# Optimization experiments

Measured on AMD Instinct MI355X. Metric: run time of the kernel, lower is better.

Reference implementation:

```python
import jax, jax.numpy as jnp
import numpy as np

N, F, FH, H = 4096, 512, 64, 8  # nodes, in-features, per-head out-features, heads
ALPHA = 0.2  # LeakyReLU slope


def setup_inputs() -> dict:
    key = jax.random.key(0)
    ks = jax.random.split(key, 6)
    X = jax.random.normal(ks[0], (N, F), dtype=jnp.float32)
    A = (jax.random.uniform(ks[1], (N, N)) < 0.02).astype(jnp.float32)
    glorot_w = (2.0 / (F + FH)) ** 0.5
    glorot_a = (2.0 / (FH + 1)) ** 0.5
    W = jax.random.normal(ks[2], (H, F, FH), dtype=jnp.float32) * glorot_w
    a_self = jax.random.normal(ks[3], (H, FH), dtype=jnp.float32) * glorot_a
    a_neigh = jax.random.normal(ks[4], (H, FH), dtype=jnp.float32) * glorot_a
    b = jnp.zeros((H, FH), dtype=jnp.float32)
    return {"X": X, "A": A, "W": W, "a_self": a_self, "a_neigh": a_neigh, "b": b}


def reference(X, A, W, a_self, a_neigh, b):
    # per-head linear projection: [H, N, FH]
    feats = jnp.einsum('nf,hfo->hno', X, W)
    s_self = jnp.einsum('hno,ho->hn', feats, a_self)    # [H, N]
    s_neigh = jnp.einsum('hno,ho->hn', feats, a_neigh)  # [H, N]
    # additive logits: self_i + neigh_j -> [H, N, N]
    dense = s_self[:, :, None] + s_neigh[:, None, :]
    dense = jnp.where(dense > 0, dense, ALPHA * dense)  # LeakyReLU(0.2)
    dense = dense * A[None, :, :]                       # multiplicative adjacency (as in source)
    attn = jax.nn.softmax(dense, axis=-1)               # full-row softmax (as in source)
    # dropout is identity at inference
    out = jnp.einsum('hij,hjo->hio', attn, feats) + b[:, None, :]  # [H, N, FH]
    out = jnp.transpose(out, (1, 0, 2)).reshape(N, H * FH)         # concat heads
    return jax.nn.relu(out)
```

## Files before the change

kernel.cpp:

```cpp
#include <hip/hip_runtime.h>
#include <hip/hip_bf16.h>

#define N_NODES 4096
#define F_IN 512
#define FHD 64
#define H_HEADS 8
#define C_OUT 512
#define ALPHA 0.2f
#define MAXE 192
#define MAXE_P 200
#define GEMM_BLOCKS 512

typedef __attribute__((ext_vector_type(8))) short bf16x8;
typedef __attribute__((ext_vector_type(4))) float f32x4;

static __device__ __forceinline__ unsigned short f2bf(float f) {
  __hip_bfloat16 h = __float2bfloat16(f);
  union { __hip_bfloat16 h; unsigned short u; } cvt;
  cvt.h = h;
  return cvt.u;
}

__global__ __launch_bounds__(256) void conv_kernel(
    const float* __restrict__ W, unsigned short* __restrict__ WbT,
    float* __restrict__ colsum) {
  __shared__ float sT[64][65];
  const int bid = blockIdx.x;
  const int tid = threadIdx.x;
  if (bid < 64) {
    const int fblk = bid & 7, h = bid >> 3;
#pragma unroll
    for (int i = 0; i < 16; ++i) {
      int idx = tid + i * 256;
      int f = idx >> 6, o = idx & 63;
      sT[f][o] = W[((size_t)h * F_IN + fblk * 64 + f) * FHD + o];
    }
    __syncthreads();
#pragma unroll
    for (int i = 0; i < 16; ++i) {
      int idx = tid + i * 256;
      int o = idx >> 6, f = idx & 63;
      WbT[(size_t)h * FHD * F_IN + (size_t)o * F_IN + fblk * 64 + f] =
          f2bf(sT[f][o]);
    }
  } else {
    colsum[tid] = 0.f;
    colsum[tid + 256] = 0.f;
  }
}

__global__ __launch_bounds__(256) void gemm_scan_kernel(
    const float* __restrict__ X, const unsigned short* __restrict__ WbT,
    const float* __restrict__ a_self, const float* __restrict__ a_neigh,
    const float* __restrict__ A,
    unsigned short* __restrict__ featsb,
    float* __restrict__ s_self, float* __restrict__ s_neigh,
    float* __restrict__ colsum,
    unsigned short* __restrict__ edges, int* __restrict__ degs) {
  __shared__ unsigned short sX[2][64 * 72];
  __shared__ unsigned short sW[2][64 * 72];
  __shared__ float sred[4][64];
  const int bid = blockIdx.x;
  const int tid = threadIdx.x;
  const int wid = tid >> 6, lane = tid & 63;

  if (bid >= GEMM_BLOCKS) {
    const int i = bid - GEMM_BLOCKS;
    int* wave_tot = reinterpret_cast<int*>(&sred[0][0]);
    const float4* __restrict__ Arow4 =
        reinterpret_cast<const float4*>(A + (size_t)i * N_NODES);
    float4 v[4];
#pragma unroll
    for (int q = 0; q < 4; ++q) v[q] = Arow4[tid * 4 + q];
    int mask16 = 0;
#pragma unroll
    for (int q = 0; q < 4; ++q) {
      mask16 |= (v[q].x != 0.f) ? (1 << (q * 4 + 0)) : 0;
      mask16 |= (v[q].y != 0.f) ? (1 << (q * 4 + 1)) : 0;
      mask16 |= (v[q].z != 0.f) ? (1 << (q * 4 + 2)) : 0;
      mask16 |= (v[q].w != 0.f) ? (1 << (q * 4 + 3)) : 0;
    }
    int cnt = __popc(mask16);
    int inc = cnt;
#pragma unroll
    for (int s = 1; s < 64; s <<= 1) {
      int t = __shfl_up(inc, s, 64);
      if (lane >= s) inc += t;
    }
    if (lane == 63) wave_tot[wid] = inc;
    __syncthreads();
    int wprefix = 0, tot = 0;
#pragma unroll
    for (int w = 0; w < 4; ++w) {
      int t = wave_tot[w];
      if (w < wid) wprefix += t;
      tot += t;
    }
    int pos = wprefix + inc - cnt;
    const int jbase = tid * 16;
    unsigned short* __restrict__ erow = edges + (size_t)i * MAXE;
    while (mask16) {
      int k = __ffs(mask16) - 1;
      mask16 &= mask16 - 1;
      if (pos < MAXE) erow[pos] = (unsigned short)(jbase + k);
      ++pos;
    }
    if (tid == 0) degs[i] = tot < MAXE ? tot : MAXE;
    return;
  }

  const int h = bid >> 6;
  const int n0 = (bid & 63) * 64;
  const int l15 = lane & 15, l4 = lane >> 4;

  const int row = tid >> 2, seg = (tid & 3) * 16;
  const float* xsrc = X + (size_t)(n0 + row) * F_IN + seg;
  const unsigned short* wsrc = WbT + ((size_t)h * FHD + row) * F_IN + seg;
  const int soff = row * 72 + seg;

  f32x4 acc[4];
#pragma unroll
  for (int j = 0; j < 4; ++j) acc[j] = (f32x4){0.f, 0.f, 0.f, 0.f};

  {
    float4 xa = *(const float4*)(xsrc);
    float4 xb = *(const float4*)(xsrc + 4);
    float4 xc = *(const float4*)(xsrc + 8);
    float4 xd = *(const float4*)(xsrc + 12);
    bf16x8 p0, p1;
    p0[0] = f2bf(xa.x); p0[1] = f2bf(xa.y); p0[2] = f2bf(xa.z); p0[3] = f2bf(xa.w);
    p0[4] = f2bf(xb.x); p0[5] = f2bf(xb.y); p0[6] = f2bf(xb.z); p0[7] = f2bf(xb.w);
    p1[0] = f2bf(xc.x); p1[1] = f2bf(xc.y); p1[2] = f2bf(xc.z); p1[3] = f2bf(xc.w);
    p1[4] = f2bf(xd.x); p1[5] = f2bf(xd.y); p1[6] = f2bf(xd.z); p1[7] = f2bf(xd.w);
    *(bf16x8*)&sX[0][soff] = p0;
    *(bf16x8*)&sX[0][soff + 8] = p1;
    *(bf16x8*)&sW[0][soff] = *(const bf16x8*)(wsrc);
    *(bf16x8*)&sW[0][soff + 8] = *(const bf16x8*)(wsrc + 8);
  }
  __syncthreads();

  int cur = 0;
  for (int s = 0; s < 8; ++s) {
    float4 xa, xb, xc, xd;
    bf16x8 pw0, pw1;
    const bool pf = (s < 7);
    if (pf) {
      const int k = (s + 1) * 64;
      xa = *(const float4*)(xsrc + k);
      xb = *(const float4*)(xsrc + k + 4);
      xc = *(const float4*)(xsrc + k + 8);
      xd = *(const float4*)(xsrc + k + 12);
      pw0 = *(const bf16x8*)(wsrc + k);
      pw1 = *(const bf16x8*)(wsrc + k + 8);
    }
#pragma unroll
    for (int kk = 0; kk < 2; ++kk) {
      bf16x8 a = *(const bf16x8*)&sX[cur][(wid * 16 + l15) * 72 + kk * 32 + l4 * 8];
#pragma unroll
      for (int tn = 0; tn < 4; ++tn) {
        bf16x8 b = *(const bf16x8*)&sW[cur][(tn * 16 + l15) * 72 + kk * 32 + l4 * 8];
        acc[tn] =
            __builtin_amdgcn_mfma_f32_16x16x32_bf16(a, b, acc[tn], 0, 0, 0);
      }
    }
    if (pf) {
      bf16x8 p0, p1;
      p0[0] = f2bf(xa.x); p0[1] = f2bf(xa.y); p0[2] = f2bf(xa.z); p0[3] = f2bf(xa.w);
      p0[4] = f2bf(xb.x); p0[5] = f2bf(xb.y); p0[6] = f2bf(xb.z); p0[7] = f2bf(xb.w);
      p1[0] = f2bf(xc.x); p1[1] = f2bf(xc.y); p1[2] = f2bf(xc.z); p1[3] = f2bf(xc.w);
      p1[4] = f2bf(xd.x); p1[5] = f2bf(xd.y); p1[6] = f2bf(xd.z); p1[7] = f2bf(xd.w);
      *(bf16x8*)&sX[cur ^ 1][soff] = p0;
      *(bf16x8*)&sX[cur ^ 1][soff + 8] = p1;
      *(bf16x8*)&sW[cur ^ 1][soff] = pw0;
      *(bf16x8*)&sW[cur ^ 1][soff + 8] = pw1;
      __syncthreads();
      cur ^= 1;
    }
  }

  float aS[4], aN[4];
#pragma unroll
  for (int tn = 0; tn < 4; ++tn) {
    aS[tn] = a_self[h * FHD + tn * 16 + l15];
    aN[tn] = a_neigh[h * FHD + tn * 16 + l15];
  }
#pragma unroll
  for (int r = 0; r < 4; ++r) {
    const int grow = n0 + wid * 16 + l4 * 4 + r;
#pragma unroll
    for (int tn = 0; tn < 4; ++tn)
      featsb[(size_t)grow * C_OUT + h * FHD + tn * 16 + l15] =
          f2bf(acc[tn][r]);
    float ps = 0.f, pn = 0.f;
#pragma unroll
    for (int tn = 0; tn < 4; ++tn) {
      float v = acc[tn][r];
      ps = fmaf(v, aS[tn], ps);
      pn = fmaf(v, aN[tn], pn);
    }
#pragma unroll
    for (int sh = 1; sh < 16; sh <<= 1) {
      ps += __shfl_xor(ps, sh, 64);
      pn += __shfl_xor(pn, sh, 64);
    }
    if (l15 == 0) {
      s_self[grow * 8 + h] = ps;
      s_neigh[grow * 8 + h] = pn;
    }
  }

  float psum[4];
#pragma unroll
  for (int tn = 0; tn < 4; ++tn) {
    float s = acc[tn][0] + acc[tn][1] + acc[tn][2] + acc[tn][3];
    s += __shfl_xor(s, 16, 64);
    s += __shfl_xor(s, 32, 64);
    psum[tn] = s;
  }
  __syncthreads();
  if (l4 == 0) {
#pragma unroll
    for (int tn = 0; tn < 4; ++tn) sred[wid][tn * 16 + l15] = psum[tn];
  }
  __syncthreads();
  if (tid < 64) {
    float s = sred[0][tid] + sred[1][tid] + sred[2][tid] + sred[3][tid];
    atomicAdd(&colsum[h * FHD + tid], s);
  }
}

__global__ __launch_bounds__(256) void attn_kernel(
    const unsigned short* __restrict__ edges, const int* __restrict__ degs,
    const unsigned short* __restrict__ featsb,
    const float* __restrict__ s_self, const float* __restrict__ s_neigh,
    const float* __restrict__ colsum, const float* __restrict__ bias,
    float* __restrict__ out) {
  const int i = blockIdx.x;
  const int tid = threadIdx.x;
  const int wid = tid >> 6, lane = tid & 63;
  __shared__ int s_idx[MAXE];
  __shared__ int s_off[MAXE];
  __shared__ float s_w[H_HEADS][MAXE_P];
  __shared__ float sh_self[8];
  __shared__ float sh_e0[8], sh_invZ[8];
  __shared__ float s_part[3][64][9];

  const int deg = degs[i];
  if (tid < 8) sh_self[tid] = s_self[i * 8 + tid];
  if (tid < deg) {
    int j = edges[(size_t)i * MAXE + tid];
    s_idx[tid] = j;
    s_off[tid] = j << 10;
  }
  __syncthreads();

  for (int k = tid; k < deg * 8; k += 256) {
    int e = k >> 3, h = k & 7;
    int j = s_idx[e];
    float l = sh_self[h] + s_neigh[j * 8 + h];
    s_w[h][e] = l > 0.f ? l : ALPHA * l;
  }
  __syncthreads();

#pragma unroll
  for (int p = 0; p < 2; ++p) {
    const int h = wid * 2 + p;
    float m = -1e30f;
    for (int e = lane; e < deg; e += 64) m = fmaxf(m, s_w[h][e]);
#pragma unroll
    for (int s = 32; s > 0; s >>= 1) m = fmaxf(m, __shfl_xor(m, s, 64));
    m = fmaxf(m, 0.0f);
    float e0 = __expf(-m);
    float zs = 0.f;
    for (int e = lane; e < deg; e += 64) {
      float w = __expf(s_w[h][e] - m);
      s_w[h][e] = w - e0;
      zs += w;
    }
#pragma unroll
    for (int s = 32; s > 0; s >>= 1) zs += __shfl_xor(zs, s, 64);
    if (lane == 0) {
      sh_e0[h] = e0;
      sh_invZ[h] = 1.0f / (zs + (float)(N_NODES - deg) * e0);
    }
  }
  __syncthreads();

  const int co = lane;
  const int q = wid;
  const int h = co >> 3;
  const int dq = (deg + 3) >> 2;
  const int ebeg = q * dq;
  const int eend = (ebeg + dq) < deg ? (ebeg + dq) : deg;
  const char* __restrict__ fbase =
      reinterpret_cast<const char*>(featsb) + co * 16;
  float a0 = 0.f, a1 = 0.f, a2 = 0.f, a3 = 0.f;
  float a4 = 0.f, a5 = 0.f, a6 = 0.f, a7 = 0.f;
  float c0 = 0.f, c1 = 0.f, c2 = 0.f, c3 = 0.f;
  float c4 = 0.f, c5 = 0.f, c6 = 0.f, c7 = 0.f;
  int e = ebeg;
  for (; e + 3 < eend; e += 4) {
    float w0 = s_w[h][e], w1 = s_w[h][e + 1];
    float w2 = s_w[h][e + 2], w3 = s_w[h][e + 3];
    int o0 = s_off[e], o1 = s_off[e + 1];
    int o2 = s_off[e + 2], o3 = s_off[e + 3];
    uint4 u0 = *reinterpret_cast<const uint4*>(fbase + o0);
    uint4 u1 = *reinterpret_cast<const uint4*>(fbase + o1);
    uint4 u2 = *reinterpret_cast<const uint4*>(fbase + o2);
    uint4 u3 = *reinterpret_cast<const uint4*>(fbase + o3);
    a0 = fmaf(w0, __uint_as_float(u0.x << 16), a0);
    a1 = fmaf(w0, __uint_as_float(u0.x & 0xFFFF0000u), a1);
    a2 = fmaf(w0, __uint_as_float(u0.y << 16), a2);
    a3 = fmaf(w0, __uint_as_float(u0.y & 0xFFFF0000u), a3);
    a4 = fmaf(w0, __uint_as_float(u0.z << 16), a4);
    a5 = fmaf(w0, __uint_as_float(u0.z & 0xFFFF0000u), a5);
    a6 = fmaf(w0, __uint_as_float(u0.w << 16), a6);
    a7 = fmaf(w0, __uint_as_float(u0.w & 0xFFFF0000u), a7);
    c0 = fmaf(w1, __uint_as_float(u1.x << 16), c0);
    c1 = fmaf(w1, __uint_as_float(u1.x & 0xFFFF0000u), c1);
    c2 = fmaf(w1, __uint_as_float(u1.y << 16), c2);
    c3 = fmaf(w1, __uint_as_float(u1.y & 0xFFFF0000u), c3);
    c4 = fmaf(w1, __uint_as_float(u1.z << 16), c4);
    c5 = fmaf(w1, __uint_as_float(u1.z & 0xFFFF0000u), c5);
    c6 = fmaf(w1, __uint_as_float(u1.w << 16), c6);
    c7 = fmaf(w1, __uint_as_float(u1.w & 0xFFFF0000u), c7);
    a0 = fmaf(w2, __uint_as_float(u2.x << 16), a0);
    a1 = fmaf(w2, __uint_as_float(u2.x & 0xFFFF0000u), a1);
    a2 = fmaf(w2, __uint_as_float(u2.y << 16), a2);
    a3 = fmaf(w2, __uint_as_float(u2.y & 0xFFFF0000u), a3);
    a4 = fmaf(w2, __uint_as_float(u2.z << 16), a4);
    a5 = fmaf(w2, __uint_as_float(u2.z & 0xFFFF0000u), a5);
    a6 = fmaf(w2, __uint_as_float(u2.w << 16), a6);
    a7 = fmaf(w2, __uint_as_float(u2.w & 0xFFFF0000u), a7);
    c0 = fmaf(w3, __uint_as_float(u3.x << 16), c0);
    c1 = fmaf(w3, __uint_as_float(u3.x & 0xFFFF0000u), c1);
    c2 = fmaf(w3, __uint_as_float(u3.y << 16), c2);
    c3 = fmaf(w3, __uint_as_float(u3.y & 0xFFFF0000u), c3);
    c4 = fmaf(w3, __uint_as_float(u3.z << 16), c4);
    c5 = fmaf(w3, __uint_as_float(u3.z & 0xFFFF0000u), c5);
    c6 = fmaf(w3, __uint_as_float(u3.w << 16), c6);
    c7 = fmaf(w3, __uint_as_float(u3.w & 0xFFFF0000u), c7);
  }
  for (; e < eend; ++e) {
    float w0 = s_w[h][e];
    uint4 u0 = *reinterpret_cast<const uint4*>(fbase + s_off[e]);
    a0 = fmaf(w0, __uint_as_float(u0.x << 16), a0);
    a1 = fmaf(w0, __uint_as_float(u0.x & 0xFFFF0000u), a1);
    a2 = fmaf(w0, __uint_as_float(u0.y << 16), a2);
    a3 = fmaf(w0, __uint_as_float(u0.y & 0xFFFF0000u), a3);
    a4 = fmaf(w0, __uint_as_float(u0.z << 16), a4);
    a5 = fmaf(w0, __uint_as_float(u0.z & 0xFFFF0000u), a5);
    a6 = fmaf(w0, __uint_as_float(u0.w << 16), a6);
    a7 = fmaf(w0, __uint_as_float(u0.w & 0xFFFF0000u), a7);
  }
  a0 += c0; a1 += c1; a2 += c2; a3 += c3;
  a4 += c4; a5 += c5; a6 += c6; a7 += c7;

  if (q > 0) {
    float* p = &s_part[q - 1][co][0];
    p[0] = a0; p[1] = a1; p[2] = a2; p[3] = a3;
    p[4] = a4; p[5] = a5; p[6] = a6; p[7] = a7;
  }
  __syncthreads();
  if (q == 0) {
#pragma unroll
    for (int pp = 0; pp < 3; ++pp) {
      const float* p = &s_part[pp][co][0];
      a0 += p[0]; a1 += p[1]; a2 += p[2]; a3 += p[3];
      a4 += p[4]; a5 += p[5]; a6 += p[6]; a7 += p[7];
    }
    const float e0 = sh_e0[h], invZ = sh_invZ[h];
    const float4 cs0 = *reinterpret_cast<const float4*>(&colsum[co * 8]);
    const float4 cs1 = *reinterpret_cast<const float4*>(&colsum[co * 8 + 4]);
    const float4 bb0 = *reinterpret_cast<const float4*>(&bias[co * 8]);
    const float4 bb1 = *reinterpret_cast<const float4*>(&bias[co * 8 + 4]);
    f32x4 o0, o1;
    float v;
    v = (a0 + e0 * cs0.x) * invZ + bb0.x; o0.x = v > 0.f ? v : 0.f;
    v = (a1 + e0 * cs0.y) * invZ + bb0.y; o0.y = v > 0.f ? v : 0.f;
    v = (a2 + e0 * cs0.z) * invZ + bb0.z; o0.z = v > 0.f ? v : 0.f;
    v = (a3 + e0 * cs0.w) * invZ + bb0.w; o0.w = v > 0.f ? v : 0.f;
    v = (a4 + e0 * cs1.x) * invZ + bb1.x; o1.x = v > 0.f ? v : 0.f;
    v = (a5 + e0 * cs1.y) * invZ + bb1.y; o1.y = v > 0.f ? v : 0.f;
    v = (a6 + e0 * cs1.z) * invZ + bb1.z; o1.z = v > 0.f ? v : 0.f;
    v = (a7 + e0 * cs1.w) * invZ + bb1.w; o1.w = v > 0.f ? v : 0.f;
    f32x4* dst = reinterpret_cast<f32x4*>(&out[(size_t)i * C_OUT + co * 8]);
    __builtin_nontemporal_store(o0, dst);
    __builtin_nontemporal_store(o1, dst + 1);
  }
}

extern "C" void kernel_launch(void* const* d_in, const int* in_sizes, int n_in,
                              void* d_out, int out_size, void* d_ws, size_t ws_size,
                              hipStream_t stream) {
  const float* X = (const float*)d_in[0];
  const float* A = (const float*)d_in[1];
  const float* W = (const float*)d_in[2];
  const float* a_self = (const float*)d_in[3];
  const float* a_neigh = (const float*)d_in[4];
  const float* b = (const float*)d_in[5];
  float* out = (float*)d_out;

  char* ws = (char*)d_ws;
  unsigned short* featsb = (unsigned short*)ws;
  char* p = ws + (size_t)N_NODES * C_OUT * 2;
  float* s_self = (float*)p;  p += N_NODES * H_HEADS * 4;
  float* s_neigh = (float*)p; p += N_NODES * H_HEADS * 4;
  float* colsum = (float*)p;  p += C_OUT * 4;
  int* degs = (int*)p;        p += N_NODES * 4;
  unsigned short* edges = (unsigned short*)p;
  p += (size_t)N_NODES * MAXE * 2;
  unsigned short* WbT = (unsigned short*)p;

  conv_kernel<<<65, 256, 0, stream>>>(W, WbT, colsum);
  gemm_scan_kernel<<<GEMM_BLOCKS + N_NODES, 256, 0, stream>>>(
      X, WbT, a_self, a_neigh, A, featsb, s_self, s_neigh, colsum, edges,
      degs);
  attn_kernel<<<N_NODES, 256, 0, stream>>>(edges, degs, featsb, s_self,
                                           s_neigh, colsum, b, out);
}
```

Measured before the change: 51.56 us.

## Split attention blocks by head half, shrink GEMM K-tile, nontemporal adjacency loads

```diff
diff --git a/kernel.cpp b/kernel.cpp
--- a/kernel.cpp
+++ b/kernel.cpp
@@ -57,8 +57,8 @@
     float* __restrict__ s_self, float* __restrict__ s_neigh,
     float* __restrict__ colsum,
     unsigned short* __restrict__ edges, int* __restrict__ degs) {
-  __shared__ unsigned short sX[2][64 * 72];
-  __shared__ unsigned short sW[2][64 * 72];
+  __shared__ unsigned short sX[2][64 * 40];
+  __shared__ unsigned short sW[2][64 * 40];
   __shared__ float sred[4][64];
   const int bid = blockIdx.x;
   const int tid = threadIdx.x;
@@ -67,11 +67,12 @@
   if (bid >= GEMM_BLOCKS) {
     const int i = bid - GEMM_BLOCKS;
     int* wave_tot = reinterpret_cast<int*>(&sred[0][0]);
-    const float4* __restrict__ Arow4 =
-        reinterpret_cast<const float4*>(A + (size_t)i * N_NODES);
-    float4 v[4];
-#pragma unroll
-    for (int q = 0; q < 4; ++q) v[q] = Arow4[tid * 4 + q];
+    const f32x4* __restrict__ Arow4 =
+        reinterpret_cast<const f32x4*>(A + (size_t)i * N_NODES);
+    f32x4 v[4];
+#pragma unroll
+    for (int q = 0; q < 4; ++q)
+      v[q] = __builtin_nontemporal_load(&Arow4[tid * 4 + q]);
     int mask16 = 0;
 #pragma unroll
     for (int q = 0; q < 4; ++q) {
@@ -113,10 +114,10 @@
   const int n0 = (bid & 63) * 64;
   const int l15 = lane & 15, l4 = lane >> 4;
 
-  const int row = tid >> 2, seg = (tid & 3) * 16;
+  const int row = tid >> 2, seg = (tid & 3) * 8;
   const float* xsrc = X + (size_t)(n0 + row) * F_IN + seg;
   const unsigned short* wsrc = WbT + ((size_t)h * FHD + row) * F_IN + seg;
-  const int soff = row * 72 + seg;
+  const int soff = row * 40 + seg;
 
   f32x4 acc[4];
 #pragma unroll
@@ -125,54 +126,38 @@
   {
     float4 xa = *(const float4*)(xsrc);
     float4 xb = *(const float4*)(xsrc + 4);
-    float4 xc = *(const float4*)(xsrc + 8);
-    float4 xd = *(const float4*)(xsrc + 12);
-    bf16x8 p0, p1;
-    p0[0] = f2bf(xa.x); p0[1] = f2bf(xa.y); p0[2] = f2bf(xa.z); p0[3] = f2bf(xa.w);
-    p0[4] = f2bf(xb.x); p0[5] = f2bf(xb.y); p0[6] = f2bf(xb.z); p0[7] = f2bf(xb.w);
-    p1[0] = f2bf(xc.x); p1[1] = f2bf(xc.y); p1[2] = f2bf(xc.z); p1[3] = f2bf(xc.w);
-    p1[4] = f2bf(xd.x); p1[5] = f2bf(xd.y); p1[6] = f2bf(xd.z); p1[7] = f2bf(xd.w);
-    *(bf16x8*)&sX[0][soff] = p0;
-    *(bf16x8*)&sX[0][soff + 8] = p1;
+    bf16x8 p;
+    p[0] = f2bf(xa.x); p[1] = f2bf(xa.y); p[2] = f2bf(xa.z); p[3] = f2bf(xa.w);
+    p[4] = f2bf(xb.x); p[5] = f2bf(xb.y); p[6] = f2bf(xb.z); p[7] = f2bf(xb.w);
+    *(bf16x8*)&sX[0][soff] = p;
     *(bf16x8*)&sW[0][soff] = *(const bf16x8*)(wsrc);
-    *(bf16x8*)&sW[0][soff + 8] = *(const bf16x8*)(wsrc + 8);
   }
   __syncthreads();
 
   int cur = 0;
-  for (int s = 0; s < 8; ++s) {
-    float4 xa, xb, xc, xd;
-    bf16x8 pw0, pw1;
-    const bool pf = (s < 7);
+  for (int s = 0; s < 16; ++s) {
+    float4 xa, xb;
+    bf16x8 pw;
+    const bool pf = (s < 15);
     if (pf) {
-      const int k = (s + 1) * 64;
+      const int k = (s + 1) * 32;
       xa = *(const float4*)(xsrc + k);
       xb = *(const float4*)(xsrc + k + 4);
-      xc = *(const float4*)(xsrc + k + 8);
-      xd = *(const float4*)(xsrc + k + 12);
-      pw0 = *(const bf16x8*)(wsrc + k);
-      pw1 = *(const bf16x8*)(wsrc + k + 8);
-    }
-#pragma unroll
-    for (int kk = 0; kk < 2; ++kk) {
-      bf16x8 a = *(const bf16x8*)&sX[cur][(wid * 16 + l15) * 72 + kk * 32 + l4 * 8];
-#pragma unroll
-      for (int tn = 0; tn < 4; ++tn) {
-        bf16x8 b = *(const bf16x8*)&sW[cur][(tn * 16 + l15) * 72 + kk * 32 + l4 * 8];
-        acc[tn] =
-            __builtin_amdgcn_mfma_f32_16x16x32_bf16(a, b, acc[tn], 0, 0, 0);
-      }
+      pw = *(const bf16x8*)(wsrc + k);
+    }
+    bf16x8 a = *(const bf16x8*)&sX[cur][(wid * 16 + l15) * 40 + l4 * 8];
+#pragma unroll
+    for (int tn = 0; tn < 4; ++tn) {
+      bf16x8 b = *(const bf16x8*)&sW[cur][(tn * 16 + l15) * 40 + l4 * 8];
+      acc[tn] =
+          __builtin_amdgcn_mfma_f32_16x16x32_bf16(a, b, acc[tn], 0, 0, 0);
     }
     if (pf) {
-      bf16x8 p0, p1;
-      p0[0] = f2bf(xa.x); p0[1] = f2bf(xa.y); p0[2] = f2bf(xa.z); p0[3] = f2bf(xa.w);
-      p0[4] = f2bf(xb.x); p0[5] = f2bf(xb.y); p0[6] = f2bf(xb.z); p0[7] = f2bf(xb.w);
-      p1[0] = f2bf(xc.x); p1[1] = f2bf(xc.y); p1[2] = f2bf(xc.z); p1[3] = f2bf(xc.w);
-      p1[4] = f2bf(xd.x); p1[5] = f2bf(xd.y); p1[6] = f2bf(xd.z); p1[7] = f2bf(xd.w);
-      *(bf16x8*)&sX[cur ^ 1][soff] = p0;
-      *(bf16x8*)&sX[cur ^ 1][soff + 8] = p1;
-      *(bf16x8*)&sW[cur ^ 1][soff] = pw0;
-      *(bf16x8*)&sW[cur ^ 1][soff + 8] = pw1;
+      bf16x8 p;
+      p[0] = f2bf(xa.x); p[1] = f2bf(xa.y); p[2] = f2bf(xa.z); p[3] = f2bf(xa.w);
+      p[4] = f2bf(xb.x); p[5] = f2bf(xb.y); p[6] = f2bf(xb.z); p[7] = f2bf(xb.w);
+      *(bf16x8*)&sX[cur ^ 1][soff] = p;
+      *(bf16x8*)&sW[cur ^ 1][soff] = pw;
       __syncthreads();
       cur ^= 1;
     }
@@ -235,18 +220,20 @@
     const float* __restrict__ s_self, const float* __restrict__ s_neigh,
     const float* __restrict__ colsum, const float* __restrict__ bias,
     float* __restrict__ out) {
-  const int i = blockIdx.x;
+  const int bid = blockIdx.x;
+  const int half = (bid & 7) >> 2;
+  const int i = (bid >> 3) * 4 + (bid & 3);
   const int tid = threadIdx.x;
   const int wid = tid >> 6, lane = tid & 63;
   __shared__ int s_idx[MAXE];
   __shared__ int s_off[MAXE];
-  __shared__ float s_w[H_HEADS][MAXE_P];
-  __shared__ float sh_self[8];
-  __shared__ float sh_e0[8], sh_invZ[8];
-  __shared__ float s_part[3][64][9];
+  __shared__ float s_w[4][MAXE_P];
+  __shared__ float sh_self[4];
+  __shared__ float sh_e0[4], sh_invZ[4];
+  __shared__ float s_part[3][64][5];
 
   const int deg = degs[i];
-  if (tid < 8) sh_self[tid] = s_self[i * 8 + tid];
+  if (tid < 4) sh_self[tid] = s_self[i * 8 + half * 4 + tid];
   if (tid < deg) {
     int j = edges[(size_t)i * MAXE + tid];
     s_idx[tid] = j;
@@ -254,139 +241,106 @@
   }
   __syncthreads();
 
-  for (int k = tid; k < deg * 8; k += 256) {
-    int e = k >> 3, h = k & 7;
+  for (int k = tid; k < deg * 4; k += 256) {
+    int e = k >> 2, h4 = k & 3;
     int j = s_idx[e];
-    float l = sh_self[h] + s_neigh[j * 8 + h];
-    s_w[h][e] = l > 0.f ? l : ALPHA * l;
-  }
-  __syncthreads();
-
-#pragma unroll
-  for (int p = 0; p < 2; ++p) {
-    const int h = wid * 2 + p;
+    float l = sh_self[h4] + s_neigh[j * 8 + half * 4 + h4];
+    s_w[h4][e] = l > 0.f ? l : ALPHA * l;
+  }
+  __syncthreads();
+
+  {
+    const int h4 = wid;
     float m = -1e30f;
-    for (int e = lane; e < deg; e += 64) m = fmaxf(m, s_w[h][e]);
+    for (int e = lane; e < deg; e += 64) m = fmaxf(m, s_w[h4][e]);
 #pragma unroll
     for (int s = 32; s > 0; s >>= 1) m = fmaxf(m, __shfl_xor(m, s, 64));
     m = fmaxf(m, 0.0f);
     float e0 = __expf(-m);
     float zs = 0.f;
     for (int e = lane; e < deg; e += 64) {
-      float w = __expf(s_w[h][e] - m);
-      s_w[h][e] = w - e0;
+      float w = __expf(s_w[h4][e] - m);
+      s_w[h4][e] = w - e0;
       zs += w;
     }
 #pragma unroll
     for (int s = 32; s > 0; s >>= 1) zs += __shfl_xor(zs, s, 64);
     if (lane == 0) {
-      sh_e0[h] = e0;
-      sh_invZ[h] = 1.0f / (zs + (float)(N_NODES - deg) * e0);
-    }
-  }
-  __syncthreads();
-
-  const int co = lane;
+      sh_e0[h4] = e0;
+      sh_invZ[h4] = 1.0f / (zs + (float)(N_NODES - deg) * e0);
+    }
+  }
+  __syncthreads();
+
+  const int h4 = lane >> 4;
   const int q = wid;
-  const int h = co >> 3;
   const int dq = (deg + 3) >> 2;
   const int ebeg = q * dq;
   const int eend = (ebeg + dq) < deg ? (ebeg + dq) : deg;
   const char* __restrict__ fbase =
-      reinterpret_cast<const char*>(featsb) + co * 16;
+      reinterpret_cast<const char*>(featsb) + half * 512 + lane * 8;
   float a0 = 0.f, a1 = 0.f, a2 = 0.f, a3 = 0.f;
-  float a4 = 0.f, a5 = 0.f, a6 = 0.f, a7 = 0.f;
   float c0 = 0.f, c1 = 0.f, c2 = 0.f, c3 = 0.f;
-  float c4 = 0.f, c5 = 0.f, c6 = 0.f, c7 = 0.f;
   int e = ebeg;
   for (; e + 3 < eend; e += 4) {
-    float w0 = s_w[h][e], w1 = s_w[h][e + 1];
-    float w2 = s_w[h][e + 2], w3 = s_w[h][e + 3];
+    float w0 = s_w[h4][e], w1 = s_w[h4][e + 1];
+    float w2 = s_w[h4][e + 2], w3 = s_w[h4][e + 3];
     int o0 = s_off[e], o1 = s_off[e + 1];
     int o2 = s_off[e + 2], o3 = s_off[e + 3];
-    uint4 u0 = *reinterpret_cast<const uint4*>(fbase + o0);
-    uint4 u1 = *reinterpret_cast<const uint4*>(fbase + o1);
-    uint4 u2 = *reinterpret_cast<const uint4*>(fbase + o2);
-    uint4 u3 = *reinterpret_cast<const uint4*>(fbase + o3);
+    uint2 u0 = *reinterpret_cast<const uint2*>(fbase + o0);
+    uint2 u1 = *reinterpret_cast<const uint2*>(fbase + o1);
+    uint2 u2 = *reinterpret_cast<const uint2*>(fbase + o2);
+    uint2 u3 = *reinterpret_cast<const uint2*>(fbase + o3);
     a0 = fmaf(w0, __uint_as_float(u0.x << 16), a0);
     a1 = fmaf(w0, __uint_as_float(u0.x & 0xFFFF0000u), a1);
     a2 = fmaf(w0, __uint_as_float(u0.y << 16), a2);
     a3 = fmaf(w0, __uint_as_float(u0.y & 0xFFFF0000u), a3);
-    a4 = fmaf(w0, __uint_as_float(u0.z << 16), a4);
-    a5 = fmaf(w0, __uint_as_float(u0.z & 0xFFFF0000u), a5);
-    a6 = fmaf(w0, __uint_as_float(u0.w << 16), a6);
-    a7 = fmaf(w0, __uint_as_float(u0.w & 0xFFFF0000u), a7);
     c0 = fmaf(w1, __uint_as_float(u1.x << 16), c0);
     c1 = fmaf(w1, __uint_as_float(u1.x & 0xFFFF0000u), c1);
     c2 = fmaf(w1, __uint_as_float(u1.y << 16), c2);
     c3 = fmaf(w1, __uint_as_float(u1.y & 0xFFFF0000u), c3);
-    c4 = fmaf(w1, __uint_as_float(u1.z << 16), c4);
-    c5 = fmaf(w1, __uint_as_float(u1.z & 0xFFFF0000u), c5);
-    c6 = fmaf(w1, __uint_as_float(u1.w << 16), c6);
-    c7 = fmaf(w1, __uint_as_float(u1.w & 0xFFFF0000u), c7);
     a0 = fmaf(w2, __uint_as_float(u2.x << 16), a0);
     a1 = fmaf(w2, __uint_as_float(u2.x & 0xFFFF0000u), a1);
     a2 = fmaf(w2, __uint_as_float(u2.y << 16), a2);
     a3 = fmaf(w2, __uint_as_float(u2.y & 0xFFFF0000u), a3);
-    a4 = fmaf(w2, __uint_as_float(u2.z << 16), a4);
-    a5 = fmaf(w2, __uint_as_float(u2.z & 0xFFFF0000u), a5);
-    a6 = fmaf(w2, __uint_as_float(u2.w << 16), a6);
-    a7 = fmaf(w2, __uint_as_float(u2.w & 0xFFFF0000u), a7);
     c0 = fmaf(w3, __uint_as_float(u3.x << 16), c0);
     c1 = fmaf(w3, __uint_as_float(u3.x & 0xFFFF0000u), c1);
     c2 = fmaf(w3, __uint_as_float(u3.y << 16), c2);
     c3 = fmaf(w3, __uint_as_float(u3.y & 0xFFFF0000u), c3);
-    c4 = fmaf(w3, __uint_as_float(u3.z << 16), c4);
-    c5 = fmaf(w3, __uint_as_float(u3.z & 0xFFFF0000u), c5);
-    c6 = fmaf(w3, __uint_as_float(u3.w << 16), c6);
-    c7 = fmaf(w3, __uint_as_float(u3.w & 0xFFFF0000u), c7);
   }
   for (; e < eend; ++e) {
-    float w0 = s_w[h][e];
-    uint4 u0 = *reinterpret_cast<const uint4*>(fbase + s_off[e]);
+    float w0 = s_w[h4][e];
+    uint2 u0 = *reinterpret_cast<const uint2*>(fbase + s_off[e]);
     a0 = fmaf(w0, __uint_as_float(u0.x << 16), a0);
     a1 = fmaf(w0, __uint_as_float(u0.x & 0xFFFF0000u), a1);
     a2 = fmaf(w0, __uint_as_float(u0.y << 16), a2);
     a3 = fmaf(w0, __uint_as_float(u0.y & 0xFFFF0000u), a3);
-    a4 = fmaf(w0, __uint_as_float(u0.z << 16), a4);
-    a5 = fmaf(w0, __uint_as_float(u0.z & 0xFFFF0000u), a5);
-    a6 = fmaf(w0, __uint_as_float(u0.w << 16), a6);
-    a7 = fmaf(w0, __uint_as_float(u0.w & 0xFFFF0000u), a7);
   }
   a0 += c0; a1 += c1; a2 += c2; a3 += c3;
-  a4 += c4; a5 += c5; a6 += c6; a7 += c7;
 
   if (q > 0) {
-    float* p = &s_part[q - 1][co][0];
+    float* p = &s_part[q - 1][lane][0];
     p[0] = a0; p[1] = a1; p[2] = a2; p[3] = a3;
-    p[4] = a4; p[5] = a5; p[6] = a6; p[7] = a7;
   }
   __syncthreads();
   if (q == 0) {
 #pragma unroll
     for (int pp = 0; pp < 3; ++pp) {
-      const float* p = &s_part[pp][co][0];
+      const float* p = &s_part[pp][lane][0];
       a0 += p[0]; a1 += p[1]; a2 += p[2]; a3 += p[3];
-      a4 += p[4]; a5 += p[5]; a6 += p[6]; a7 += p[7];
-    }
-    const float e0 = sh_e0[h], invZ = sh_invZ[h];
-    const float4 cs0 = *reinterpret_cast<const float4*>(&colsum[co * 8]);
-    const float4 cs1 = *reinterpret_cast<const float4*>(&colsum[co * 8 + 4]);
-    const float4 bb0 = *reinterpret_cast<const float4*>(&bias[co * 8]);
-    const float4 bb1 = *reinterpret_cast<const float4*>(&bias[co * 8 + 4]);
-    f32x4 o0, o1;
+    }
+    const int gc = half * 256 + lane * 4;
+    const float e0 = sh_e0[h4], invZ = sh_invZ[h4];
+    const float4 cs = *reinterpret_cast<const float4*>(&colsum[gc]);
+    const float4 bb = *reinterpret_cast<const float4*>(&bias[gc]);
+    f32x4 o;
     float v;
-    v = (a0 + e0 * cs0.x) * invZ + bb0.x; o0.x = v > 0.f ? v : 0.f;
-    v = (a1 + e0 * cs0.y) * invZ + bb0.y; o0.y = v > 0.f ? v : 0.f;
-    v = (a2 + e0 * cs0.z) * invZ + bb0.z; o0.z = v > 0.f ? v : 0.f;
-    v = (a3 + e0 * cs0.w) * invZ + bb0.w; o0.w = v > 0.f ? v : 0.f;
-    v = (a4 + e0 * cs1.x) * invZ + bb1.x; o1.x = v > 0.f ? v : 0.f;
-    v = (a5 + e0 * cs1.y) * invZ + bb1.y; o1.y = v > 0.f ? v : 0.f;
-    v = (a6 + e0 * cs1.z) * invZ + bb1.z; o1.z = v > 0.f ? v : 0.f;
-    v = (a7 + e0 * cs1.w) * invZ + bb1.w; o1.w = v > 0.f ? v : 0.f;
-    f32x4* dst = reinterpret_cast<f32x4*>(&out[(size_t)i * C_OUT + co * 8]);
-    __builtin_nontemporal_store(o0, dst);
-    __builtin_nontemporal_store(o1, dst + 1);
+    v = (a0 + e0 * cs.x) * invZ + bb.x; o.x = v > 0.f ? v : 0.f;
+    v = (a1 + e0 * cs.y) * invZ + bb.y; o.y = v > 0.f ? v : 0.f;
+    v = (a2 + e0 * cs.z) * invZ + bb.z; o.z = v > 0.f ? v : 0.f;
+    v = (a3 + e0 * cs.w) * invZ + bb.w; o.w = v > 0.f ? v : 0.f;
+    f32x4* dst = reinterpret_cast<f32x4*>(&out[(size_t)i * C_OUT + gc]);
+    __builtin_nontemporal_store(o, dst);
   }
 }
 
@@ -416,6 +370,6 @@
   gemm_scan_kernel<<<GEMM_BLOCKS + N_NODES, 256, 0, stream>>>(
       X, WbT, a_self, a_neigh, A, featsb, s_self, s_neigh, colsum, edges,
       degs);
-  attn_kernel<<<N_NODES, 256, 0, stream>>>(edges, degs, featsb, s_self,
-                                           s_neigh, colsum, b, out);
-}
+  attn_kernel<<<N_NODES * 2, 256, 0, stream>>>(edges, degs, featsb, s_self,
+                                               s_neigh, colsum, b, out);
+}
```

Result: slower. 66.75 us (+29.5%).

## Split attention aggregation across two blocks per node by head halves

Applied to the files above, without the earlier changes.

```diff
diff --git a/kernel.cpp b/kernel.cpp
--- a/kernel.cpp
+++ b/kernel.cpp
@@ -235,18 +235,20 @@
     const float* __restrict__ s_self, const float* __restrict__ s_neigh,
     const float* __restrict__ colsum, const float* __restrict__ bias,
     float* __restrict__ out) {
-  const int i = blockIdx.x;
+  const int bid = blockIdx.x;
+  const int half = (bid & 7) >> 2;
+  const int i = (bid >> 3) * 4 + (bid & 3);
   const int tid = threadIdx.x;
   const int wid = tid >> 6, lane = tid & 63;
   __shared__ int s_idx[MAXE];
   __shared__ int s_off[MAXE];
-  __shared__ float s_w[H_HEADS][MAXE_P];
-  __shared__ float sh_self[8];
-  __shared__ float sh_e0[8], sh_invZ[8];
-  __shared__ float s_part[3][64][9];
+  __shared__ float s_w[4][MAXE_P];
+  __shared__ float sh_self[4];
+  __shared__ float sh_e0[4], sh_invZ[4];
+  __shared__ float s_part[7][32][9];
 
   const int deg = degs[i];
-  if (tid < 8) sh_self[tid] = s_self[i * 8 + tid];
+  if (tid < 4) sh_self[tid] = s_self[i * 8 + half * 4 + tid];
   if (tid < deg) {
     int j = edges[(size_t)i * MAXE + tid];
     s_idx[tid] = j;
@@ -254,60 +256,57 @@
   }
   __syncthreads();
 
-  for (int k = tid; k < deg * 8; k += 256) {
-    int e = k >> 3, h = k & 7;
+  for (int k = tid; k < deg * 4; k += 256) {
+    int e = k >> 2, h4 = k & 3;
     int j = s_idx[e];
-    float l = sh_self[h] + s_neigh[j * 8 + h];
-    s_w[h][e] = l > 0.f ? l : ALPHA * l;
-  }
-  __syncthreads();
-
-#pragma unroll
-  for (int p = 0; p < 2; ++p) {
-    const int h = wid * 2 + p;
+    float l = sh_self[h4] + s_neigh[j * 8 + half * 4 + h4];
+    s_w[h4][e] = l > 0.f ? l : ALPHA * l;
+  }
+  __syncthreads();
+
+  {
+    const int h4 = wid;
     float m = -1e30f;
-    for (int e = lane; e < deg; e += 64) m = fmaxf(m, s_w[h][e]);
+    for (int e = lane; e < deg; e += 64) m = fmaxf(m, s_w[h4][e]);
 #pragma unroll
     for (int s = 32; s > 0; s >>= 1) m = fmaxf(m, __shfl_xor(m, s, 64));
     m = fmaxf(m, 0.0f);
     float e0 = __expf(-m);
     float zs = 0.f;
     for (int e = lane; e < deg; e += 64) {
-      float w = __expf(s_w[h][e] - m);
-      s_w[h][e] = w - e0;
+      float w = __expf(s_w[h4][e] - m);
+      s_w[h4][e] = w - e0;
       zs += w;
     }
 #pragma unroll
     for (int s = 32; s > 0; s >>= 1) zs += __shfl_xor(zs, s, 64);
     if (lane == 0) {
-      sh_e0[h] = e0;
-      sh_invZ[h] = 1.0f / (zs + (float)(N_NODES - deg) * e0);
-    }
-  }
-  __syncthreads();
-
-  const int co = lane;
+      sh_e0[h4] = e0;
+      sh_invZ[h4] = 1.0f / (zs + (float)(N_NODES - deg) * e0);
+    }
+  }
+  __syncthreads();
+
+  const int sub = lane >> 5;
+  const int cl = lane & 31;
+  const int h4 = cl >> 3;
   const int q = wid;
-  const int h = co >> 3;
   const int dq = (deg + 3) >> 2;
   const int ebeg = q * dq;
   const int eend = (ebeg + dq) < deg ? (ebeg + dq) : deg;
   const char* __restrict__ fbase =
-      reinterpret_cast<const char*>(featsb) + co * 16;
+      reinterpret_cast<const char*>(featsb) + half * 512 + cl * 16;
   float a0 = 0.f, a1 = 0.f, a2 = 0.f, a3 = 0.f;
   float a4 = 0.f, a5 = 0.f, a6 = 0.f, a7 = 0.f;
   float c0 = 0.f, c1 = 0.f, c2 = 0.f, c3 = 0.f;
   float c4 = 0.f, c5 = 0.f, c6 = 0.f, c7 = 0.f;
   int e = ebeg;
   for (; e + 3 < eend; e += 4) {
-    float w0 = s_w[h][e], w1 = s_w[h][e + 1];
-    float w2 = s_w[h][e + 2], w3 = s_w[h][e + 3];
-    int o0 = s_off[e], o1 = s_off[e + 1];
-    int o2 = s_off[e + 2], o3 = s_off[e + 3];
+    float w0 = s_w[h4][e + sub];
+    float w1 = s_w[h4][e + 2 + sub];
+    int o0 = s_off[e + sub], o1 = s_off[e + 2 + sub];
     uint4 u0 = *reinterpret_cast<const uint4*>(fbase + o0);
     uint4 u1 = *reinterpret_cast<const uint4*>(fbase + o1);
-    uint4 u2 = *reinterpret_cast<const uint4*>(fbase + o2);
-    uint4 u3 = *reinterpret_cast<const uint4*>(fbase + o3);
     a0 = fmaf(w0, __uint_as_float(u0.x << 16), a0);
     a1 = fmaf(w0, __uint_as_float(u0.x & 0xFFFF0000u), a1);
     a2 = fmaf(w0, __uint_as_float(u0.y << 16), a2);
@@ -324,26 +323,10 @@
     c5 = fmaf(w1, __uint_as_float(u1.z & 0xFFFF0000u), c5);
     c6 = fmaf(w1, __uint_as_float(u1.w << 16), c6);
     c7 = fmaf(w1, __uint_as_float(u1.w & 0xFFFF0000u), c7);
-    a0 = fmaf(w2, __uint_as_float(u2.x << 16), a0);
-    a1 = fmaf(w2, __uint_as_float(u2.x & 0xFFFF0000u), a1);
-    a2 = fmaf(w2, __uint_as_float(u2.y << 16), a2);
-    a3 = fmaf(w2, __uint_as_float(u2.y & 0xFFFF0000u), a3);
-    a4 = fmaf(w2, __uint_as_float(u2.z << 16), a4);
-    a5 = fmaf(w2, __uint_as_float(u2.z & 0xFFFF0000u), a5);
-    a6 = fmaf(w2, __uint_as_float(u2.w << 16), a6);
-    a7 = fmaf(w2, __uint_as_float(u2.w & 0xFFFF0000u), a7);
-    c0 = fmaf(w3, __uint_as_float(u3.x << 16), c0);
-    c1 = fmaf(w3, __uint_as_float(u3.x & 0xFFFF0000u), c1);
-    c2 = fmaf(w3, __uint_as_float(u3.y << 16), c2);
-    c3 = fmaf(w3, __uint_as_float(u3.y & 0xFFFF0000u), c3);
-    c4 = fmaf(w3, __uint_as_float(u3.z << 16), c4);
-    c5 = fmaf(w3, __uint_as_float(u3.z & 0xFFFF0000u), c5);
-    c6 = fmaf(w3, __uint_as_float(u3.w << 16), c6);
-    c7 = fmaf(w3, __uint_as_float(u3.w & 0xFFFF0000u), c7);
-  }
-  for (; e < eend; ++e) {
-    float w0 = s_w[h][e];
-    uint4 u0 = *reinterpret_cast<const uint4*>(fbase + s_off[e]);
+  }
+  for (; e + sub < eend; e += 2) {
+    float w0 = s_w[h4][e + sub];
+    uint4 u0 = *reinterpret_cast<const uint4*>(fbase + s_off[e + sub]);
     a0 = fmaf(w0, __uint_as_float(u0.x << 16), a0);
     a1 = fmaf(w0, __uint_as_float(u0.x & 0xFFFF0000u), a1);
     a2 = fmaf(w0, __uint_as_float(u0.y << 16), a2);
@@ -356,24 +339,26 @@
   a0 += c0; a1 += c1; a2 += c2; a3 += c3;
   a4 += c4; a5 += c5; a6 += c6; a7 += c7;
 
-  if (q > 0) {
-    float* p = &s_part[q - 1][co][0];
+  const int pidx = q * 2 + sub;
+  if (pidx > 0) {
+    float* p = &s_part[pidx - 1][cl][0];
     p[0] = a0; p[1] = a1; p[2] = a2; p[3] = a3;
     p[4] = a4; p[5] = a5; p[6] = a6; p[7] = a7;
   }
   __syncthreads();
-  if (q == 0) {
-#pragma unroll
-    for (int pp = 0; pp < 3; ++pp) {
-      const float* p = &s_part[pp][co][0];
+  if (pidx == 0) {
+#pragma unroll
+    for (int pp = 0; pp < 7; ++pp) {
+      const float* p = &s_part[pp][cl][0];
       a0 += p[0]; a1 += p[1]; a2 += p[2]; a3 += p[3];
       a4 += p[4]; a5 += p[5]; a6 += p[6]; a7 += p[7];
     }
-    const float e0 = sh_e0[h], invZ = sh_invZ[h];
-    const float4 cs0 = *reinterpret_cast<const float4*>(&colsum[co * 8]);
-    const float4 cs1 = *reinterpret_cast<const float4*>(&colsum[co * 8 + 4]);
-    const float4 bb0 = *reinterpret_cast<const float4*>(&bias[co * 8]);
-    const float4 bb1 = *reinterpret_cast<const float4*>(&bias[co * 8 + 4]);
+    const int gc = half * 256 + cl * 8;
+    const float e0 = sh_e0[h4], invZ = sh_invZ[h4];
+    const float4 cs0 = *reinterpret_cast<const float4*>(&colsum[gc]);
+    const float4 cs1 = *reinterpret_cast<const float4*>(&colsum[gc + 4]);
+    const float4 bb0 = *reinterpret_cast<const float4*>(&bias[gc]);
+    const float4 bb1 = *reinterpret_cast<const float4*>(&bias[gc + 4]);
     f32x4 o0, o1;
     float v;
     v = (a0 + e0 * cs0.x) * invZ + bb0.x; o0.x = v > 0.f ? v : 0.f;
@@ -384,7 +369,7 @@
     v = (a5 + e0 * cs1.y) * invZ + bb1.y; o1.y = v > 0.f ? v : 0.f;
     v = (a6 + e0 * cs1.z) * invZ + bb1.z; o1.z = v > 0.f ? v : 0.f;
     v = (a7 + e0 * cs1.w) * invZ + bb1.w; o1.w = v > 0.f ? v : 0.f;
-    f32x4* dst = reinterpret_cast<f32x4*>(&out[(size_t)i * C_OUT + co * 8]);
+    f32x4* dst = reinterpret_cast<f32x4*>(&out[(size_t)i * C_OUT + gc]);
     __builtin_nontemporal_store(o0, dst);
     __builtin_nontemporal_store(o1, dst + 1);
   }
@@ -416,6 +401,6 @@
   gemm_scan_kernel<<<GEMM_BLOCKS + N_NODES, 256, 0, stream>>>(
       X, WbT, a_self, a_neigh, A, featsb, s_self, s_neigh, colsum, edges,
       degs);
-  attn_kernel<<<N_NODES, 256, 0, stream>>>(edges, degs, featsb, s_self,
-                                           s_neigh, colsum, b, out);
+  attn_kernel<<<N_NODES * 2, 256, 0, stream>>>(edges, degs, featsb, s_self,
+                                               s_neigh, colsum, b, out);
 }
```

Result: slower. 55.07 us (+6.8%).

## Fold weight conversion into gemm_scan kernel with a global readiness flag

Applied to the files above, without the earlier changes.

```diff
diff --git a/kernel.cpp b/kernel.cpp
--- a/kernel.cpp
+++ b/kernel.cpp
@@ -21,52 +21,49 @@
   return cvt.u;
 }
 
-__global__ __launch_bounds__(256) void conv_kernel(
-    const float* __restrict__ W, unsigned short* __restrict__ WbT,
-    float* __restrict__ colsum) {
-  __shared__ float sT[64][65];
-  const int bid = blockIdx.x;
-  const int tid = threadIdx.x;
-  if (bid < 64) {
-    const int fblk = bid & 7, h = bid >> 3;
-#pragma unroll
-    for (int i = 0; i < 16; ++i) {
-      int idx = tid + i * 256;
-      int f = idx >> 6, o = idx & 63;
-      sT[f][o] = W[((size_t)h * F_IN + fblk * 64 + f) * FHD + o];
-    }
-    __syncthreads();
-#pragma unroll
-    for (int i = 0; i < 16; ++i) {
-      int idx = tid + i * 256;
-      int o = idx >> 6, f = idx & 63;
-      WbT[(size_t)h * FHD * F_IN + (size_t)o * F_IN + fblk * 64 + f] =
-          f2bf(sT[f][o]);
-    }
-  } else {
-    colsum[tid] = 0.f;
-    colsum[tid + 256] = 0.f;
-  }
-}
-
 __global__ __launch_bounds__(256) void gemm_scan_kernel(
-    const float* __restrict__ X, const unsigned short* __restrict__ WbT,
+    const float* __restrict__ X, const float* __restrict__ W,
+    unsigned short* __restrict__ WbT,
     const float* __restrict__ a_self, const float* __restrict__ a_neigh,
     const float* __restrict__ A,
     unsigned short* __restrict__ featsb,
     float* __restrict__ s_self, float* __restrict__ s_neigh,
     float* __restrict__ colsum,
-    unsigned short* __restrict__ edges, int* __restrict__ degs) {
-  __shared__ unsigned short sX[2][64 * 72];
-  __shared__ unsigned short sW[2][64 * 72];
-  __shared__ float sred[4][64];
+    unsigned short* __restrict__ edges, int* __restrict__ degs,
+    int* __restrict__ wflag) {
+  __shared__ __align__(16) unsigned char smem[19456];
   const int bid = blockIdx.x;
   const int tid = threadIdx.x;
   const int wid = tid >> 6, lane = tid & 63;
 
   if (bid >= GEMM_BLOCKS) {
     const int i = bid - GEMM_BLOCKS;
-    int* wave_tot = reinterpret_cast<int*>(&sred[0][0]);
+
+    if (i < 64) {
+      float (*sT)[65] = reinterpret_cast<float(*)[65]>(smem);
+      const int fblk = i & 7, h = i >> 3;
+#pragma unroll
+      for (int k = 0; k < 16; ++k) {
+        int idx = tid + k * 256;
+        int f = idx >> 6, o = idx & 63;
+        sT[f][o] = W[((size_t)h * F_IN + fblk * 64 + f) * FHD + o];
+      }
+      __syncthreads();
+#pragma unroll
+      for (int k = 0; k < 16; ++k) {
+        int idx = tid + k * 256;
+        int o = idx >> 6, f = idx & 63;
+        WbT[(size_t)h * FHD * F_IN + (size_t)o * F_IN + fblk * 64 + f] =
+            f2bf(sT[f][o]);
+      }
+      __syncthreads();
+      if (tid == 0)
+        __hip_atomic_fetch_add(wflag, 1, __ATOMIC_RELEASE,
+                               __HIP_MEMORY_SCOPE_AGENT);
+      __syncthreads();
+    }
+
+    int* wave_tot = reinterpret_cast<int*>(smem + 18432);
     const float4* __restrict__ Arow4 =
         reinterpret_cast<const float4*>(A + (size_t)i * N_NODES);
     float4 v[4];
@@ -109,6 +106,17 @@
     return;
   }
 
+  unsigned short* sX = reinterpret_cast<unsigned short*>(smem);
+  unsigned short* sW = reinterpret_cast<unsigned short*>(smem + 9216);
+  float (*sred)[64] = reinterpret_cast<float(*)[64]>(smem + 18432);
+
+  if (tid == 0) {
+    while (__hip_atomic_load(wflag, __ATOMIC_ACQUIRE,
+                             __HIP_MEMORY_SCOPE_AGENT) < 64) {
+    }
+  }
+  __syncthreads();
+
   const int h = bid >> 6;
   const int n0 = (bid & 63) * 64;
   const int l15 = lane & 15, l4 = lane >> 4;
@@ -122,29 +130,28 @@
 #pragma unroll
   for (int j = 0; j < 4; ++j) acc[j] = (f32x4){0.f, 0.f, 0.f, 0.f};
 
-  {
-    float4 xa = *(const float4*)(xsrc);
-    float4 xb = *(const float4*)(xsrc + 4);
-    float4 xc = *(const float4*)(xsrc + 8);
-    float4 xd = *(const float4*)(xsrc + 12);
-    bf16x8 p0, p1;
-    p0[0] = f2bf(xa.x); p0[1] = f2bf(xa.y); p0[2] = f2bf(xa.z); p0[3] = f2bf(xa.w);
-    p0[4] = f2bf(xb.x); p0[5] = f2bf(xb.y); p0[6] = f2bf(xb.z); p0[7] = f2bf(xb.w);
-    p1[0] = f2bf(xc.x); p1[1] = f2bf(xc.y); p1[2] = f2bf(xc.z); p1[3] = f2bf(xc.w);
-    p1[4] = f2bf(xd.x); p1[5] = f2bf(xd.y); p1[6] = f2bf(xd.z); p1[7] = f2bf(xd.w);
-    *(bf16x8*)&sX[0][soff] = p0;
-    *(bf16x8*)&sX[0][soff + 8] = p1;
-    *(bf16x8*)&sW[0][soff] = *(const bf16x8*)(wsrc);
-    *(bf16x8*)&sW[0][soff + 8] = *(const bf16x8*)(wsrc + 8);
-  }
-  __syncthreads();
-
-  int cur = 0;
+  float4 xa = *(const float4*)(xsrc);
+  float4 xb = *(const float4*)(xsrc + 4);
+  float4 xc = *(const float4*)(xsrc + 8);
+  float4 xd = *(const float4*)(xsrc + 12);
+  bf16x8 pw0 = *(const bf16x8*)(wsrc);
+  bf16x8 pw1 = *(const bf16x8*)(wsrc + 8);
+
   for (int s = 0; s < 8; ++s) {
-    float4 xa, xb, xc, xd;
-    bf16x8 pw0, pw1;
-    const bool pf = (s < 7);
-    if (pf) {
+    __syncthreads();
+    {
+      bf16x8 p0, p1;
+      p0[0] = f2bf(xa.x); p0[1] = f2bf(xa.y); p0[2] = f2bf(xa.z); p0[3] = f2bf(xa.w);
+      p0[4] = f2bf(xb.x); p0[5] = f2bf(xb.y); p0[6] = f2bf(xb.z); p0[7] = f2bf(xb.w);
+      p1[0] = f2bf(xc.x); p1[1] = f2bf(xc.y); p1[2] = f2bf(xc.z); p1[3] = f2bf(xc.w);
+      p1[4] = f2bf(xd.x); p1[5] = f2bf(xd.y); p1[6] = f2bf(xd.z); p1[7] = f2bf(xd.w);
+      *(bf16x8*)&sX[soff] = p0;
+      *(bf16x8*)&sX[soff + 8] = p1;
+      *(bf16x8*)&sW[soff] = pw0;
+      *(bf16x8*)&sW[soff + 8] = pw1;
+    }
+    __syncthreads();
+    if (s < 7) {
       const int k = (s + 1) * 64;
       xa = *(const float4*)(xsrc + k);
       xb = *(const float4*)(xsrc + k + 4);
@@ -155,26 +162,13 @@
     }
 #pragma unroll
     for (int kk = 0; kk < 2; ++kk) {
-      bf16x8 a = *(const bf16x8*)&sX[cur][(wid * 16 + l15) * 72 + kk * 32 + l4 * 8];
+      bf16x8 a = *(const bf16x8*)&sX[(wid * 16 + l15) * 72 + kk * 32 + l4 * 8];
 #pragma unroll
       for (int tn = 0; tn < 4; ++tn) {
-        bf16x8 b = *(const bf16x8*)&sW[cur][(tn * 16 + l15) * 72 + kk * 32 + l4 * 8];
+        bf16x8 b = *(const bf16x8*)&sW[(tn * 16 + l15) * 72 + kk * 32 + l4 * 8];
         acc[tn] =
             __builtin_amdgcn_mfma_f32_16x16x32_bf16(a, b, acc[tn], 0, 0, 0);
       }
-    }
-    if (pf) {
-      bf16x8 p0, p1;
-      p0[0] = f2bf(xa.x); p0[1] = f2bf(xa.y); p0[2] = f2bf(xa.z); p0[3] = f2bf(xa.w);
-      p0[4] = f2bf(xb.x); p0[5] = f2bf(xb.y); p0[6] = f2bf(xb.z); p0[7] = f2bf(xb.w);
-      p1[0] = f2bf(xc.x); p1[1] = f2bf(xc.y); p1[2] = f2bf(xc.z); p1[3] = f2bf(xc.w);
-      p1[4] = f2bf(xd.x); p1[5] = f2bf(xd.y); p1[6] = f2bf(xd.z); p1[7] = f2bf(xd.w);
-      *(bf16x8*)&sX[cur ^ 1][soff] = p0;
-      *(bf16x8*)&sX[cur ^ 1][soff + 8] = p1;
-      *(bf16x8*)&sW[cur ^ 1][soff] = pw0;
-      *(bf16x8*)&sW[cur ^ 1][soff + 8] = pw1;
-      __syncthreads();
-      cur ^= 1;
     }
   }
 
@@ -407,15 +401,16 @@
   float* s_self = (float*)p;  p += N_NODES * H_HEADS * 4;
   float* s_neigh = (float*)p; p += N_NODES * H_HEADS * 4;
   float* colsum = (float*)p;  p += C_OUT * 4;
+  int* wflag = (int*)p;       p += 16;
   int* degs = (int*)p;        p += N_NODES * 4;
   unsigned short* edges = (unsigned short*)p;
   p += (size_t)N_NODES * MAXE * 2;
   unsigned short* WbT = (unsigned short*)p;
 
-  conv_kernel<<<65, 256, 0, stream>>>(W, WbT, colsum);
+  hipMemsetAsync(colsum, 0, C_OUT * 4 + 16, stream);
   gemm_scan_kernel<<<GEMM_BLOCKS + N_NODES, 256, 0, stream>>>(
-      X, WbT, a_self, a_neigh, A, featsb, s_self, s_neigh, colsum, edges,
-      degs);
+      X, W, WbT, a_self, a_neigh, A, featsb, s_self, s_neigh, colsum, edges,
+      degs, wflag);
   attn_kernel<<<N_NODES, 256, 0, stream>>>(edges, degs, featsb, s_self,
                                            s_neigh, colsum, b, out);
 }
```

After: 78.41 us. 52.1% more time.
